# Performance work log

Measured on AMD Instinct MI355X. Metric: run time of the kernel, lower is better.

The kernel has to match this reference:

```python
import jax, jax.numpy as jnp
import numpy as np

N = 50000      # entity nodes
E = 300000     # edges in edge_index_all (and edge_index)
E_LINE = 50000 # line-graph edges over relations
EH = 128       # e_hidden
RH = 64        # r_hidden
REL1 = 2000
REL2 = 2000
GH = 3 * EH + RH  # GAT hidden = 448


def seg_softmax(e, idx, n):
    # torch_geometric softmax: exp(e - segmax[idx]) / (segsum + 1e-16)
    m = jax.ops.segment_max(e, idx, num_segments=n)
    ex = jnp.exp(e - m[idx])
    s = jax.ops.segment_sum(ex, idx, num_segments=n)
    return ex / (s[idx] + 1e-16)


def setup_inputs() -> dict:
    key = jax.random.key(0)
    ks = jax.random.split(key, 24)

    def nrm(k, shape, s=0.1):
        return jax.random.normal(k, shape, dtype=jnp.float32) * s

    # edges without self loops: dst = (src + off) % N, off in [1, N)
    src = jax.random.randint(ks[0], (E,), 0, N)
    off = jax.random.randint(ks[1], (E,), 1, N)
    edge_index_all = jnp.stack([src, (src + off) % N])
    src2 = jax.random.randint(ks[2], (E,), 0, N)
    off2 = jax.random.randint(ks[3], (E,), 1, N)
    edge_index = jnp.stack([src2, (src2 + off2) % N])

    rel = jax.random.randint(ks[4], (E,), 0, REL1)
    rel_all = jax.random.randint(ks[5], (E,), 0, 2 * REL1)
    line_graph_index_out = jax.random.randint(ks[6], (2, E_LINE), 0, REL1)
    line_graph_index_in = jax.random.randint(ks[7], (2, E_LINE), 0, REL1)

    return {
        "x_e": nrm(ks[8], (N, EH), 1.0),
        "rel_emb1": nrm(ks[9], (REL1, RH), 1.0),
        "rel_emb2": nrm(ks[10], (REL2, RH), 1.0),
        "w_gcn1": nrm(ks[11], (EH, EH)),
        "Wh1": nrm(ks[12], (EH, EH)),
        "bh1": nrm(ks[13], (EH,)),
        "w_gcn2": nrm(ks[14], (EH, EH)),
        "Wh2": nrm(ks[15], (EH, EH)),
        "bh2": nrm(ks[16], (EH,)),
        "ai_l": nrm(ks[17], (RH,)),
        "aj_l": nrm(ks[18], (RH,)),
        "w_tw": nrm(ks[19], (2 * EH + RH,)),
        "ai_g": nrm(ks[20], (GH,)),
        "aj_g": nrm(ks[21], (GH,)),
        "ar_g": nrm(ks[22], (RH,)),
        "edge_index": edge_index,
        "rel": rel,
        "edge_index_all": edge_index_all,
        "rel_all": rel_all,
        "line_graph_index_out": line_graph_index_out,
        "line_graph_index_in": line_graph_index_in,
    }


def mrea_forward(x_e, rel_emb1, w_gcn1, Wh1, bh1, w_gcn2, Wh2, bh2,
                 ai_l, aj_l, w_tw, ai_g, aj_g, ar_g,
                 edge_index_all, rel_all, lg_out, lg_in):
    n = x_e.shape[0]
    # GCN/GAT unpack: edge_index_j, edge_index_i = edge_index (row0=j, row1=i)
    j, i = edge_index_all[0], edge_index_all[1]

    def gcn(x, W):
        deg = jax.ops.segment_sum(jnp.ones(i.shape, x.dtype), i, num_segments=n)
        dinv = jnp.where(deg > 0, deg ** -0.5, 0.0)
        norm = dinv[j] * dinv[i]  # [E]
        agg = jax.nn.relu(jax.ops.segment_sum(norm[:, None] * x[j], i, num_segments=n))
        return agg @ W.T

    def highway(x1, x2, W, b):
        g = jax.nn.sigmoid(x1 @ W.T + b)
        return g * x2 + (1.0 - g) * x1

    x = highway(x_e, gcn(x_e, w_gcn1), Wh1, bh1)
    x = highway(x, gcn(x, w_gcn2), Wh2, bh2)

    # L_GAT over relation line graphs (softmax grouped by edge_index_j, as in source)
    nr = rel_emb1.shape[0]
    def l_gat(xr, ei):
        jj, ii = ei[0], ei[1]
        e = (xr @ ai_l)[ii] + (xr @ aj_l)[jj]
        alpha = seg_softmax(jax.nn.leaky_relu(e), jj, nr)
        return jax.nn.relu(jax.ops.segment_sum(alpha[:, None] * xr[jj], ii, num_segments=nr))

    rel_emb = jnp.concatenate([l_gat(rel_emb1, lg_out), l_gat(rel_emb1, lg_in)], axis=0)  # [2*REL1, RH]

    # T-wise attention: edge_index_i, edge_index_j = edge_index_all (row0=i, row1=j)
    ti, tj = edge_index_all[0], edge_index_all[1]
    feat = jnp.concatenate([x[ti], rel_emb[rel_all], x[tj]], axis=1)  # [E, 2e+r]
    att = seg_softmax(feat @ w_tw, ti, n)
    x_agg = jax.nn.relu(jax.ops.segment_sum(feat * att[:, None], ti, num_segments=n))
    x_rel = jnp.concatenate([x, x_agg], axis=1)  # [N, 3e+r]

    # GAT on x_rel with relation bias (row0=j, row1=i)
    e = (x_rel @ ai_g)[i] + (x_rel @ aj_g)[j] + (rel_emb @ ar_g)[rel_all]
    alpha = seg_softmax(jax.nn.leaky_relu(e), i, n)
    gat_out = jax.nn.relu(jax.ops.segment_sum(alpha[:, None] * x_rel[j], i, num_segments=n))

    return jnp.concatenate([x_rel, gat_out], axis=1)  # [N, 2*(3e+r)]


def reference(x_e, rel_emb1, rel_emb2, w_gcn1, Wh1, bh1, w_gcn2, Wh2, bh2,
              ai_l, aj_l, w_tw, ai_g, aj_g, ar_g,
              edge_index, rel, edge_index_all, rel_all,
              line_graph_index_out, line_graph_index_in):
    # Branch rel.max()+1 == rel1_size is true for our data -> rel_emb1 used.
    # rel_emb2, edge_index, rel do not enter the computation on this branch.
    return mrea_forward(x_e, rel_emb1, w_gcn1, Wh1, bh1, w_gcn2, Wh2, bh2,
                        ai_l, aj_l, w_tw, ai_g, aj_g, ar_g,
                        edge_index_all, rel_all,
                        line_graph_index_out, line_graph_index_in)
```

## Files before the change

kernel.cpp:

```cpp
#include <hip/hip_runtime.h>
#include <math.h>

#define NN 50000
#define EE 300000
#define EL 50000
#define EH 128
#define RH 64
#define R1 2000
#define NR2 4000
#define OD 896
#define NT64 782
#define GCNB 12500
#define CAP 32
#define LGCAP 64

using f32x4 = __attribute__((ext_vector_type(4))) float;
using bf16x8 = __attribute__((ext_vector_type(8))) short;

__device__ __forceinline__ float leaky(float x) { return x >= 0.f ? x : 0.01f * x; }

__device__ __forceinline__ void atomicMaxF(float* addr, float val) {
    if (val >= 0.f) atomicMax((int*)addr, __float_as_int(val));
    else            atomicMin((unsigned int*)addr, __float_as_uint(val));
}

__device__ __forceinline__ short bfrn(float f) {
    unsigned u = __float_as_uint(f);
    return (short)((u + 0x7FFFu + ((u >> 16) & 1u)) >> 16);
}
__device__ __forceinline__ void cvt1(float f, short& h, short& l) {
    h = bfrn(f);
    float hf = __uint_as_float(((unsigned)(unsigned short)h) << 16);
    l = bfrn(f - hf);
}
__device__ __forceinline__ void cvt8(float4 a, float4 b, bf16x8& hi, bf16x8& lo) {
    float v[8] = {a.x, a.y, a.z, a.w, b.x, b.y, b.z, b.w};
#pragma unroll
    for (int e = 0; e < 8; ++e) {
        short h, l;
        cvt1(v[e], h, l);
        hi[e] = h;
        lo[e] = l;
    }
}

__device__ __forceinline__ float2 bf2f(unsigned u) {
    float2 f;
    f.x = __uint_as_float(u << 16);
    f.y = __uint_as_float(u & 0xFFFF0000u);
    return f;
}
__device__ __forceinline__ float bf1f(unsigned short u) {
    return __uint_as_float(((unsigned)u) << 16);
}
__device__ __forceinline__ unsigned packbf(float a, float b) {
    return (unsigned)(unsigned short)bfrn(a) | (((unsigned)(unsigned short)bfrn(b)) << 16);
}

__global__ __launch_bounds__(256) void k_sij(const float* __restrict__ rel1,
                                             const float* __restrict__ ai_l, const float* __restrict__ aj_l,
                                             float* __restrict__ s_i, float* __restrict__ s_j) {
    int r = blockIdx.x * 256 + threadIdx.x;
    if (r < R1) {
        const float* m = rel1 + (long)r * 64;
        float a = 0.f, bb = 0.f;
#pragma unroll
        for (int c = 0; c < 64; ++c) {
            float v = m[c];
            a += v * ai_l[c];
            bb += v * aj_l[c];
        }
        s_i[r] = a;
        s_j[r] = bb;
    }
}

__global__ void k_fill_all(const int* __restrict__ e0, const int* __restrict__ e1,
                           const int* __restrict__ rel_all,
                           int* __restrict__ cnt0, int* __restrict__ cnt1,
                           int2* __restrict__ csr0p, int2* __restrict__ csr1p,
                           const int* __restrict__ lgo, const int* __restrict__ lgi,
                           const float* __restrict__ s_i, const float* __restrict__ s_j,
                           float* __restrict__ lgsc, float* __restrict__ lgmax,
                           int* __restrict__ lgcnt, int* __restrict__ lgsrc,
                           int* __restrict__ lgpos,
                           const float* __restrict__ W0, const float* __restrict__ W1,
                           const float* __restrict__ W2, const float* __restrict__ W3,
                           float* __restrict__ P0, float* __restrict__ P1,
                           float* __restrict__ P2, float* __restrict__ P3) {
    if (blockIdx.x < 32) {
        int slot = blockIdx.x * 256 + threadIdx.x;
        int m = slot >> 11;
        int rem = slot & 2047;
        int kb = rem >> 9;
        int nt = (rem >> 6) & 7;
        int l = rem & 63;
        const float* W = m == 0 ? W0 : m == 1 ? W1 : m == 2 ? W2 : W3;
        float* P = m == 0 ? P0 : m == 1 ? P1 : m == 2 ? P2 : P3;
        int n = (nt << 4) + (l & 15);
        int k0 = (kb << 5) + ((l >> 4) << 2);
        float4 a0 = *(const float4*)(W + (n << 7) + k0);
        float4 a1 = *(const float4*)(W + (n << 7) + k0 + 16);
        bf16x8 hv, lv;
        cvt8(a0, a1, hv, lv);
        int u = ((kb << 3) + nt) * 64 + l;
        *(bf16x8*)(P + ((long)u << 2)) = hv;
        *(bf16x8*)(P + 8192 + ((long)u << 2)) = lv;
        return;
    }
    int gid = (blockIdx.x - 32) * blockDim.x + threadIdx.x;
    int stride = (gridDim.x - 32) * blockDim.x;
    for (int i = gid; i < EE; i += stride) {
        int j0 = e0[i], i1 = e1[i], ra = rel_all[i];
        int p = atomicAdd(&cnt0[j0], 1);
        if (p < CAP) csr0p[(j0 << 5) + p] = make_int2(i1, ra);
        int q = atomicAdd(&cnt1[i1], 1);
        if (q < CAP) csr1p[(i1 << 5) + q] = make_int2(j0, ra);
    }
    for (int e = gid; e < 2 * EL; e += stride) {
        int g1 = e >= EL;
        int ee = g1 ? e - EL : e;
        const int* L = g1 ? lgi : lgo;
        int jj = L[ee], ii = L[ee + EL];
        float v = leaky(s_j[jj] + s_i[ii]);
        lgsc[e] = v;
        atomicMaxF(&lgmax[(g1 ? R1 : 0) + jj], v);
        int g = (g1 ? R1 : 0) + ii;
        int p = atomicAdd(&lgcnt[g], 1);
        if (p < LGCAP) {
            lgsrc[(g << 6) + p] = jj;
            lgpos[e] = (g << 6) + p;
        } else {
            lgpos[e] = -1;
        }
    }
}

template <bool RELU>
__device__ __forceinline__ void mfma_phase(const float* __restrict__ A, const float* __restrict__ P,
                                           float4* lds4, int tid, int l, int arow, f32x4 (&acc)[8]) {
#pragma unroll
    for (int s = 0; s < 2; ++s) {
        const float* Ap = A + ((long)arow << 7) + (s << 6) + ((l >> 4) << 2);
        float4 a0 = *(const float4*)(Ap);
        float4 a1 = *(const float4*)(Ap + 16);
        float4 a2 = *(const float4*)(Ap + 32);
        float4 a3 = *(const float4*)(Ap + 48);
        if (RELU) {
            a0.x = fmaxf(a0.x, 0.f); a0.y = fmaxf(a0.y, 0.f); a0.z = fmaxf(a0.z, 0.f); a0.w = fmaxf(a0.w, 0.f);
            a1.x = fmaxf(a1.x, 0.f); a1.y = fmaxf(a1.y, 0.f); a1.z = fmaxf(a1.z, 0.f); a1.w = fmaxf(a1.w, 0.f);
            a2.x = fmaxf(a2.x, 0.f); a2.y = fmaxf(a2.y, 0.f); a2.z = fmaxf(a2.z, 0.f); a2.w = fmaxf(a2.w, 0.f);
            a3.x = fmaxf(a3.x, 0.f); a3.y = fmaxf(a3.y, 0.f); a3.z = fmaxf(a3.z, 0.f); a3.w = fmaxf(a3.w, 0.f);
        }
        __syncthreads();
        const float4* srcH = (const float4*)P + (s << 10);
        const float4* srcL = (const float4*)P + 2048 + (s << 10);
#pragma unroll
        for (int i = 0; i < 4; ++i) {
            lds4[(i << 8) + tid] = srcH[(i << 8) + tid];
            lds4[1024 + (i << 8) + tid] = srcL[(i << 8) + tid];
        }
        __syncthreads();
        bf16x8 ah0, al0, ah1, al1;
        cvt8(a0, a1, ah0, al0);
        cvt8(a2, a3, ah1, al1);
        const bf16x8* BH = (const bf16x8*)lds4;
        const bf16x8* BL = BH + 1024;
#pragma unroll
        for (int nt = 0; nt < 8; ++nt) {
            bf16x8 bh0 = BH[(nt << 6) + l];
            bf16x8 bl0 = BL[(nt << 6) + l];
            bf16x8 bh1 = BH[512 + (nt << 6) + l];
            bf16x8 bl1 = BL[512 + (nt << 6) + l];
            f32x4 c = acc[nt];
            c = __builtin_amdgcn_mfma_f32_16x16x32_bf16(ah0, bh0, c, 0, 0, 0);
            c = __builtin_amdgcn_mfma_f32_16x16x32_bf16(al0, bh0, c, 0, 0, 0);
            c = __builtin_amdgcn_mfma_f32_16x16x32_bf16(ah0, bl0, c, 0, 0, 0);
            c = __builtin_amdgcn_mfma_f32_16x16x32_bf16(ah1, bh1, c, 0, 0, 0);
            c = __builtin_amdgcn_mfma_f32_16x16x32_bf16(al1, bh1, c, 0, 0, 0);
            c = __builtin_amdgcn_mfma_f32_16x16x32_bf16(ah1, bl1, c, 0, 0, 0);
            acc[nt] = c;
        }
    }
}

template <bool XB>
__global__ __launch_bounds__(256) void k_gcn_mfma(const float* __restrict__ Agg, const float* __restrict__ Xin,
                                                  float* __restrict__ Xout,
                                                  const float* __restrict__ Pg, const float* __restrict__ Ph,
                                                  const float* __restrict__ b,
                                                  const float* __restrict__ wtw192, float* __restrict__ xb,
                                                  unsigned short* __restrict__ xm) {
    __shared__ float4 lds4[2048];
    const int tid = threadIdx.x;
    const int l = tid & 63;
    const int wv = tid >> 6;
    const int l15 = l & 15;
    const int l4 = l >> 4;
    const int rowbase = blockIdx.x * 64 + (wv << 4);
    int arow = rowbase + l15;
    if (arow >= NN) arow = NN - 1;
    f32x4 tAcc[8], hAcc[8];
#pragma unroll
    for (int nt = 0; nt < 8; ++nt) {
        tAcc[nt] = {0.f, 0.f, 0.f, 0.f};
        hAcc[nt] = {0.f, 0.f, 0.f, 0.f};
    }
    mfma_phase<true>(Agg, Pg, lds4, tid, l, arow, tAcc);
    mfma_phase<false>(Xin, Ph, lds4, tid, l, arow, hAcc);
    const int r0 = rowbase + (l4 << 2);
    float xbp[4] = {0.f, 0.f, 0.f, 0.f};
#pragma unroll
    for (int nt = 0; nt < 8; ++nt) {
        float bv = b[(nt << 4) + l15];
#pragma unroll
        for (int r = 0; r < 4; ++r) {
            int row = r0 + r;
            if (row < NN) {
                long off = ((long)row << 7) + (nt << 4) + l15;
                float xv = Xin[off];
                float g = 1.f / (1.f + expf(-(hAcc[nt][r] + bv)));
                float ov = g * tAcc[nt][r] + (1.f - g) * xv;
                Xout[off] = ov;
                if (XB) {
                    xbp[r] += ov * wtw192[(nt << 4) + l15];
                    xm[off] = (unsigned short)bfrn(ov);
                }
            }
        }
    }
    if (XB) {
#pragma unroll
        for (int r = 0; r < 4; ++r) {
#pragma unroll
            for (int off = 1; off < 16; off <<= 1) xbp[r] += __shfl_xor(xbp[r], off);
            int row = r0 + r;
            if (l15 == 0 && row < NN) xb[row] = xbp[r];
        }
    }
}

template <int MODE>
__global__ __launch_bounds__(256) void k_gcn_gather(const int2* __restrict__ csr1p, const int* __restrict__ cnt1,
                                                    const float* __restrict__ x, float* __restrict__ agg,
                                                    const int* __restrict__ lgo, const int* __restrict__ lgi,
                                                    const float* __restrict__ lgsc, const float* __restrict__ lgmax,
                                                    float* __restrict__ lgsum,
                                                    const int* __restrict__ lgpos, float* __restrict__ lgscp,
                                                    const int* __restrict__ lgcnt, const int* __restrict__ lgsrc,
                                                    const float* __restrict__ rel1, float* __restrict__ relemb,
                                                    const float* __restrict__ wtw, const float* __restrict__ arg,
                                                    float* __restrict__ rw, float* __restrict__ gr) {
    if (blockIdx.x < GCNB) {
        int w = blockIdx.x * 4 + (threadIdx.x >> 6);
        int lane = threadIdx.x & 63;
        int cw = cnt1[w];
        int deg = cw > CAP ? CAP : cw;
        int b = w << 5;
        float dd = cw > 0 ? rsqrtf((float)cw) : 0.f;
        int sidx = 0;
        float wt = 0.f;
        if (lane < deg) {
            sidx = csr1p[b + lane].x;
            int cs = cnt1[sidx];
            wt = dd * (cs > 0 ? rsqrtf((float)cs) : 0.f);
        }
        const float2* x2 = (const float2*)x;
        float2 aA = {0.f, 0.f}, aB = {0.f, 0.f}, aC = {0.f, 0.f}, aD = {0.f, 0.f};
        int j = 0;
        for (; j + 3 < deg; j += 4) {
            int s0 = __shfl(sidx, j), s1 = __shfl(sidx, j + 1);
            int s2 = __shfl(sidx, j + 2), s3 = __shfl(sidx, j + 3);
            float w0 = __shfl(wt, j), w1 = __shfl(wt, j + 1);
            float w2 = __shfl(wt, j + 2), w3 = __shfl(wt, j + 3);
            float2 v0 = x2[((long)s0 << 6) + lane];
            float2 v1 = x2[((long)s1 << 6) + lane];
            float2 v2 = x2[((long)s2 << 6) + lane];
            float2 v3 = x2[((long)s3 << 6) + lane];
            aA.x += w0 * v0.x; aA.y += w0 * v0.y;
            aB.x += w1 * v1.x; aB.y += w1 * v1.y;
            aC.x += w2 * v2.x; aC.y += w2 * v2.y;
            aD.x += w3 * v3.x; aD.y += w3 * v3.y;
        }
        for (; j < deg; ++j) {
            int s0 = __shfl(sidx, j);
            float w0 = __shfl(wt, j);
            float2 v0 = x2[((long)s0 << 6) + lane];
            aA.x += w0 * v0.x; aA.y += w0 * v0.y;
        }
        float2 r;
        r.x = (aA.x + aB.x) + (aC.x + aD.x);
        r.y = (aA.y + aB.y) + (aC.y + aD.y);
        ((float2*)agg)[((long)w << 6) + lane] = r;
        return;
    }
    if (MODE == 1) {
        int gid = (blockIdx.x - GCNB) * 256 + threadIdx.x;
        const int stride = 391 * 256;
        for (int e = gid; e < 2 * EL; e += stride) {
            int g1 = e >= EL;
            int ee = g1 ? e - EL : e;
            const int* L = g1 ? lgi : lgo;
            int jjg = (g1 ? R1 : 0) + L[ee];
            float ex = expf(lgsc[e] - lgmax[jjg]);
            int lp = lgpos[e];
            if (lp >= 0) lgscp[lp] = ex;
            atomicAdd(&lgsum[jjg], ex);
        }
    } else {
        int d = (blockIdx.x - GCNB) * 4 + (threadIdx.x >> 6);
        int lane = threadIdx.x & 63;
        if (d >= NR2) return;
        int base = d >= R1 ? R1 : 0;
        int cd = lgcnt[d];
        int deg = cd > LGCAP ? LGCAP : cd;
        int b = d << 6;
        int src = 0;
        float al = 0.f;
        if (lane < deg) {
            src = lgsrc[b + lane];
            al = lgscp[b + lane] / (lgsum[base + src] + 1e-16f);
        }
        float aA = 0.f, aB = 0.f;
        int j = 0;
        for (; j + 1 < deg; j += 2) {
            float a0 = __shfl(al, j), a1 = __shfl(al, j + 1);
            int s0 = __shfl(src, j), s1 = __shfl(src, j + 1);
            aA += a0 * rel1[((long)s0 << 6) + lane];
            aB += a1 * rel1[((long)s1 << 6) + lane];
        }
        if (j < deg) {
            float a0 = __shfl(al, j);
            int s0 = __shfl(src, j);
            aA += a0 * rel1[((long)s0 << 6) + lane];
        }
        float v = fmaxf(aA + aB, 0.f);
        relemb[((long)d << 6) + lane] = v;
        float pa = v * wtw[128 + lane];
        float pb = v * arg[lane];
        for (int off = 32; off > 0; off >>= 1) {
            pa += __shfl_down(pa, off);
            pb += __shfl_down(pb, off);
        }
        if (lane == 0) { rw[d] = pa; gr[d] = pb; }
    }
}

__global__ __launch_bounds__(256) void k_tw_gather(const int2* __restrict__ csr0p, const int* __restrict__ cnt0,
                                                   const float* __restrict__ xb, const float* __restrict__ rw,
                                                   const float* __restrict__ x, const unsigned short* __restrict__ xm,
                                                   const float* __restrict__ relemb,
                                                   const float* __restrict__ aig, const float* __restrict__ ajg,
                                                   float* __restrict__ out,
                                                   float* __restrict__ ga, float* __restrict__ gb,
                                                   unsigned short* __restrict__ ym) {
    int w = (blockIdx.x * blockDim.x + threadIdx.x) >> 6;
    int lane = threadIdx.x & 63;
    if (w >= NN) return;
    int cw = cnt0[w];
    int deg = cw > CAP ? CAP : cw;
    int b = w << 5;
    int trx = 0, trr = 0;
    float v = -INFINITY;
    if (lane < deg) {
        int2 tr = csr0p[b + lane];
        trx = tr.x; trr = tr.y;
        v = xb[trx] + rw[trr];
    }
    float m = v;
#pragma unroll
    for (int off = 32; off > 0; off >>= 1) m = fmaxf(m, __shfl_xor(m, off));
    float al = (lane < deg) ? expf(v - m) : 0.f;
    float sum = al;
#pragma unroll
    for (int off = 32; off > 0; off >>= 1) sum += __shfl_xor(sum, off);
    const float2* x2 = (const float2*)x;
    int c2 = 2 * lane;
    float2 xt = x2[((long)w << 6) + lane];
    float a2A = 0.f, a2B = 0.f;
    float2 a3A = {0.f, 0.f}, a3B = {0.f, 0.f};
    int j = 0;
    for (; j + 3 < deg; j += 4) {
        float al0 = __shfl(al, j), al1 = __shfl(al, j + 1);
        float al2 = __shfl(al, j + 2), al3 = __shfl(al, j + 3);
        int x0i = __shfl(trx, j), x1i = __shfl(trx, j + 1);
        int x2i = __shfl(trx, j + 2), x3i = __shfl(trx, j + 3);
        int y0i = __shfl(trr, j), y1i = __shfl(trr, j + 1);
        int y2i = __shfl(trr, j + 2), y3i = __shfl(trr, j + 3);
        float r0 = relemb[((long)y0i << 6) + lane];
        float r1 = relemb[((long)y1i << 6) + lane];
        float r2 = relemb[((long)y2i << 6) + lane];
        float r3 = relemb[((long)y3i << 6) + lane];
        float2 v0 = bf2f(*(const unsigned*)(xm + ((long)x0i << 7) + c2));
        float2 v1 = bf2f(*(const unsigned*)(xm + ((long)x1i << 7) + c2));
        float2 v2 = bf2f(*(const unsigned*)(xm + ((long)x2i << 7) + c2));
        float2 v3 = bf2f(*(const unsigned*)(xm + ((long)x3i << 7) + c2));
        a2A += al0 * r0 + al1 * r1;
        a2B += al2 * r2 + al3 * r3;
        a3A.x += al0 * v0.x + al1 * v1.x;  a3A.y += al0 * v0.y + al1 * v1.y;
        a3B.x += al2 * v2.x + al3 * v3.x;  a3B.y += al2 * v2.y + al3 * v3.y;
    }
    for (; j < deg; ++j) {
        float alA = __shfl(al, j);
        int xA = __shfl(trx, j);
        int yA = __shfl(trr, j);
        a2A += alA * relemb[((long)yA << 6) + lane];
        float2 xvA = bf2f(*(const unsigned*)(xm + ((long)xA << 7) + c2));
        a3A.x += alA * xvA.x; a3A.y += alA * xvA.y;
    }
    float r = 1.f / (sum + 1e-16f);
    float sr = sum * r;
    float2 v23;
    v23.x = fmaxf(xt.x * sr, 0.f);
    v23.y = fmaxf(xt.y * sr, 0.f);
    float v4 = fmaxf((a2A + a2B) * r, 0.f);
    float2 v56;
    v56.x = fmaxf((a3A.x + a3B.x) * r, 0.f);
    v56.y = fmaxf((a3A.y + a3B.y) * r, 0.f);
    float* o = out + (long)w * OD;
    *(float2*)(o + c2) = xt;
    *(float2*)(o + 128 + c2) = v23;
    o[256 + lane] = v4;
    *(float2*)(o + 320 + c2) = v56;
    unsigned short* yr = ym + (long)w * 192;
    yr[lane] = (unsigned short)bfrn(v4);
    *(unsigned*)(yr + 64 + c2) = packbf(v56.x, v56.y);
    float da = xt.x * aig[c2] + xt.y * aig[c2 + 1] + v23.x * aig[128 + c2] + v23.y * aig[129 + c2] +
               v4 * aig[256 + lane] + v56.x * aig[320 + c2] + v56.y * aig[321 + c2];
    float db = xt.x * ajg[c2] + xt.y * ajg[c2 + 1] + v23.x * ajg[128 + c2] + v23.y * ajg[129 + c2] +
               v4 * ajg[256 + lane] + v56.x * ajg[320 + c2] + v56.y * ajg[321 + c2];
    for (int off = 32; off > 0; off >>= 1) {
        da += __shfl_down(da, off);
        db += __shfl_down(db, off);
    }
    if (lane == 0) { ga[w] = da; gb[w] = db; }
}

__global__ __launch_bounds__(256) void k_gat_gather(const int2* __restrict__ csr1p, const int* __restrict__ cnt1,
                                                    const float* __restrict__ ga, const float* __restrict__ gb,
                                                    const float* __restrict__ gr,
                                                    const unsigned short* __restrict__ xm,
                                                    const unsigned short* __restrict__ ym,
                                                    float* __restrict__ out) {
    int w = (blockIdx.x * blockDim.x + threadIdx.x) >> 6;
    int lane = threadIdx.x & 63;
    if (w >= NN) return;
    int cw = cnt1[w];
    int deg = cw > CAP ? CAP : cw;
    int b = w << 5;
    float gaw = ga[w];
    int px = 0;
    float v = -INFINITY;
    if (lane < deg) {
        int2 p = csr1p[b + lane];
        px = p.x;
        v = leaky(gaw + gb[px] + gr[p.y]);
    }
    float m = v;
#pragma unroll
    for (int off = 32; off > 0; off >>= 1) m = fmaxf(m, __shfl_xor(m, off));
    float al = (lane < deg) ? expf(v - m) : 0.f;
    float sum = al;
#pragma unroll
    for (int off = 32; off > 0; off >>= 1) sum += __shfl_xor(sum, off);
    int c2 = 2 * lane;
    float2 c0A = {0.f, 0.f}, c0B = {0.f, 0.f};
    float2 c2A = {0.f, 0.f}, c2B = {0.f, 0.f};
    float  c4A = 0.f, c4B = 0.f;
    float2 c5A = {0.f, 0.f}, c5B = {0.f, 0.f};
    int j = 0;
    for (; j + 3 < deg; j += 4) {
        float al0 = __shfl(al, j), al1 = __shfl(al, j + 1);
        float al2 = __shfl(al, j + 2), al3 = __shfl(al, j + 3);
        int p0 = __shfl(px, j), p1 = __shfl(px, j + 1);
        int p2 = __shfl(px, j + 2), p3 = __shfl(px, j + 3);
        const unsigned short* y0 = ym + (long)p0 * 192;
        const unsigned short* y1 = ym + (long)p1 * 192;
        const unsigned short* y2 = ym + (long)p2 * 192;
        const unsigned short* y3 = ym + (long)p3 * 192;
        float2 x0 = bf2f(*(const unsigned*)(xm + ((long)p0 << 7) + c2));
        float2 x1v = bf2f(*(const unsigned*)(xm + ((long)p1 << 7) + c2));
        float2 x2v = bf2f(*(const unsigned*)(xm + ((long)p2 << 7) + c2));
        float2 x3v = bf2f(*(const unsigned*)(xm + ((long)p3 << 7) + c2));
        float yv0 = bf1f(y0[lane]), yv1 = bf1f(y1[lane]);
        float yv2 = bf1f(y2[lane]), yv3 = bf1f(y3[lane]);
        float2 z0 = bf2f(*(const unsigned*)(y0 + 64 + c2));
        float2 z1 = bf2f(*(const unsigned*)(y1 + 64 + c2));
        float2 z2 = bf2f(*(const unsigned*)(y2 + 64 + c2));
        float2 z3 = bf2f(*(const unsigned*)(y3 + 64 + c2));
        c0A.x += al0 * x0.x + al1 * x1v.x;   c0A.y += al0 * x0.y + al1 * x1v.y;
        c0B.x += al2 * x2v.x + al3 * x3v.x;  c0B.y += al2 * x2v.y + al3 * x3v.y;
        c2A.x += al0 * fmaxf(x0.x, 0.f) + al1 * fmaxf(x1v.x, 0.f);
        c2A.y += al0 * fmaxf(x0.y, 0.f) + al1 * fmaxf(x1v.y, 0.f);
        c2B.x += al2 * fmaxf(x2v.x, 0.f) + al3 * fmaxf(x3v.x, 0.f);
        c2B.y += al2 * fmaxf(x2v.y, 0.f) + al3 * fmaxf(x3v.y, 0.f);
        c4A += al0 * yv0 + al1 * yv1;
        c4B += al2 * yv2 + al3 * yv3;
        c5A.x += al0 * z0.x + al1 * z1.x;  c5A.y += al0 * z0.y + al1 * z1.y;
        c5B.x += al2 * z2.x + al3 * z3.x;  c5B.y += al2 * z2.y + al3 * z3.y;
    }
    for (; j < deg; ++j) {
        float al0 = __shfl(al, j);
        int p0 = __shfl(px, j);
        const unsigned short* y0 = ym + (long)p0 * 192;
        float2 xv = bf2f(*(const unsigned*)(xm + ((long)p0 << 7) + c2));
        float yv = bf1f(y0[lane]);
        float2 zv = bf2f(*(const unsigned*)(y0 + 64 + c2));
        c0B.x += al0 * xv.x; c0B.y += al0 * xv.y;
        c2B.x += al0 * fmaxf(xv.x, 0.f); c2B.y += al0 * fmaxf(xv.y, 0.f);
        c4B += al0 * yv;
        c5B.x += al0 * zv.x; c5B.y += al0 * zv.y;
    }
    float r = 1.f / (sum + 1e-16f);
    float* o = out + (long)w * OD + 448;
    float2 w0, w2, w5;
    w0.x = fmaxf((c0A.x + c0B.x) * r, 0.f);
    w0.y = fmaxf((c0A.y + c0B.y) * r, 0.f);
    w2.x = fmaxf((c2A.x + c2B.x) * r, 0.f);
    w2.y = fmaxf((c2A.y + c2B.y) * r, 0.f);
    w5.x = fmaxf((c5A.x + c5B.x) * r, 0.f);
    w5.y = fmaxf((c5A.y + c5B.y) * r, 0.f);
    *(float2*)(o + c2) = w0;
    *(float2*)(o + 128 + c2) = w2;
    o[256 + lane] = fmaxf((c4A + c4B) * r, 0.f);
    *(float2*)(o + 320 + c2) = w5;
}

static inline int gs(long n) {
    long b = (n + 255) / 256;
    return (int)(b > 8192 ? 8192 : b);
}

extern "C" void kernel_launch(void* const* d_in, const int* in_sizes, int n_in,
                              void* d_out, int out_size, void* d_ws, size_t ws_size,
                              hipStream_t stream) {
    (void)in_sizes; (void)n_in; (void)out_size; (void)ws_size;

    const float* x_e   = (const float*)d_in[0];
    const float* rel1  = (const float*)d_in[1];
    const float* wgcn1 = (const float*)d_in[3];
    const float* Wh1   = (const float*)d_in[4];
    const float* bh1   = (const float*)d_in[5];
    const float* wgcn2 = (const float*)d_in[6];
    const float* Wh2   = (const float*)d_in[7];
    const float* bh2   = (const float*)d_in[8];
    const float* ai_l  = (const float*)d_in[9];
    const float* aj_l  = (const float*)d_in[10];
    const float* w_tw  = (const float*)d_in[11];
    const float* ai_g  = (const float*)d_in[12];
    const float* aj_g  = (const float*)d_in[13];
    const float* ar_g  = (const float*)d_in[14];
    const int* eia     = (const int*)d_in[17];
    const int* rel_all = (const int*)d_in[18];
    const int* lgo     = (const int*)d_in[19];
    const int* lgi     = (const int*)d_in[20];

    const int* e0 = eia;
    const int* e1 = eia + EE;

    float* out = (float*)d_out;
    float* ws  = (float*)d_ws;

    float* x1     = ws + 0;
    float* agg    = ws + 6400000;
    float* relemb = ws + 12800000;
    float* lgsum  = ws + 13056000;
    int*   cnt0   = (int*)(ws + 13060000);
    int*   cnt1   = (int*)(ws + 13110000);
    int*   lgcnt  = (int*)(ws + 13160000);
    float* lgmax  = ws + 13164000;
    float* xb     = ws + 13218000;
    float* rw     = ws + 13268000;
    float* gr     = ws + 13272000;
    float* ga     = ws + 13276000;
    float* gb     = ws + 13326000;
    int2*  csr0p  = (int2*)(ws + 13376000);
    int2*  csr1p  = (int2*)(ws + 16576000);
    float* wt1    = ws + 19776000;
    float* wt2    = ws + 19792384;
    float* wt3    = ws + 19808768;
    float* wt4    = ws + 19825152;
    float* s_i    = ws + 19841536;
    float* s_j    = ws + 19843536;
    float* lgsc   = ws + 19845536;
    float* lgscp  = ws + 19945536;
    int*   lgsrc  = (int*)(ws + 20201536);
    int*   lgpos  = (int*)(ws + 20457536);
    unsigned short* xm = (unsigned short*)(ws + 20557536);
    unsigned short* ym = (unsigned short*)(ws + 23757536);

    hipMemsetAsync(lgsum, 0, (size_t)112000 * sizeof(float), stream);
    k_sij<<<8, 256, 0, stream>>>(rel1, ai_l, aj_l, s_i, s_j);

    k_fill_all<<<gs(EE) + 32, 256, 0, stream>>>(e0, e1, rel_all, cnt0, cnt1, csr0p, csr1p,
                                                lgo, lgi, s_i, s_j, lgsc, lgmax, lgcnt, lgsrc, lgpos,
                                                wgcn1, Wh1, wgcn2, Wh2, wt1, wt2, wt3, wt4);

    k_gcn_gather<1><<<GCNB + 391, 256, 0, stream>>>(csr1p, cnt1, x_e, agg,
                                                    lgo, lgi, lgsc, lgmax, lgsum,
                                                    lgpos, lgscp, lgcnt, lgsrc, rel1, relemb,
                                                    w_tw, ar_g, rw, gr);
    k_gcn_mfma<false><<<NT64, 256, 0, stream>>>(agg, x_e, x1, wt1, wt2, bh1, nullptr, nullptr, nullptr);

    k_gcn_gather<2><<<GCNB + 1000, 256, 0, stream>>>(csr1p, cnt1, x1, agg,
                                                     lgo, lgi, lgsc, lgmax, lgsum,
                                                     lgpos, lgscp, lgcnt, lgsrc, rel1, relemb,
                                                     w_tw, ar_g, rw, gr);
    k_gcn_mfma<true><<<NT64, 256, 0, stream>>>(agg, x1, x1, wt3, wt4, bh2, w_tw + 192, xb, xm);

    k_tw_gather<<<12500, 256, 0, stream>>>(csr0p, cnt0, xb, rw, x1, xm, relemb, ai_g, aj_g, out, ga, gb, ym);

    k_gat_gather<<<12500, 256, 0, stream>>>(csr1p, cnt1, ga, gb, gr, xm, ym, out);
}
```

Before: 317.6 us.

## Fuse memset into pre-kernel, move csr0 build into gather, bf16 relemb, 512-thread blocks

Replaces the memset plus s_ij kernel with one kernel that also zeroes the lgsum region. Moves the csr0 CSR construction out of the fill kernel into extra blocks of the first GCN gather, so it overlaps with the gather work. Stores the relation embedding as bf16 to shrink the gather reads in the triple-wise kernel. Doubles block size to 512 threads (8 waves) for the gather kernels. The bf16 relation embedding adds rounding error, and the larger blocks may change occupancy.

```diff
diff --git a/kernel.cpp b/kernel.cpp
--- a/kernel.cpp
+++ b/kernel.cpp
@@ -10,7 +10,10 @@
 #define NR2 4000
 #define OD 896
 #define NT64 782
-#define GCNB 12500
+#define GB 6250
+#define LG1B 196
+#define C0B 600
+#define LG2B 500
 #define CAP 32
 #define LGCAP 64
 
@@ -57,28 +60,34 @@
     return (unsigned)(unsigned short)bfrn(a) | (((unsigned)(unsigned short)bfrn(b)) << 16);
 }
 
-__global__ __launch_bounds__(256) void k_sij(const float* __restrict__ rel1,
-                                             const float* __restrict__ ai_l, const float* __restrict__ aj_l,
-                                             float* __restrict__ s_i, float* __restrict__ s_j) {
-    int r = blockIdx.x * 256 + threadIdx.x;
-    if (r < R1) {
-        const float* m = rel1 + (long)r * 64;
-        float a = 0.f, bb = 0.f;
-#pragma unroll
-        for (int c = 0; c < 64; ++c) {
-            float v = m[c];
-            a += v * ai_l[c];
-            bb += v * aj_l[c];
-        }
-        s_i[r] = a;
-        s_j[r] = bb;
-    }
+__global__ __launch_bounds__(256) void k_pre0(const float* __restrict__ rel1,
+                                              const float* __restrict__ ai_l, const float* __restrict__ aj_l,
+                                              float* __restrict__ s_i, float* __restrict__ s_j,
+                                              float* __restrict__ zbase) {
+    int b = blockIdx.x, tid = threadIdx.x;
+    if (b < 8) {
+        int r = b * 256 + tid;
+        if (r < R1) {
+            const float* m = rel1 + (long)r * 64;
+            float a = 0.f, bb = 0.f;
+#pragma unroll
+            for (int c = 0; c < 64; ++c) {
+                float v = m[c];
+                a += v * ai_l[c];
+                bb += v * aj_l[c];
+            }
+            s_i[r] = a;
+            s_j[r] = bb;
+        }
+        return;
+    }
+    int idx = (b - 8) * 1024 + tid * 4;
+    if (idx < 112000) *(float4*)(zbase + idx) = make_float4(0.f, 0.f, 0.f, 0.f);
 }
 
 __global__ void k_fill_all(const int* __restrict__ e0, const int* __restrict__ e1,
                            const int* __restrict__ rel_all,
-                           int* __restrict__ cnt0, int* __restrict__ cnt1,
-                           int2* __restrict__ csr0p, int2* __restrict__ csr1p,
+                           int* __restrict__ cnt1, int2* __restrict__ csr1p,
                            const int* __restrict__ lgo, const int* __restrict__ lgi,
                            const float* __restrict__ s_i, const float* __restrict__ s_j,
                            float* __restrict__ lgsc, float* __restrict__ lgmax,
@@ -112,8 +121,6 @@
     int stride = (gridDim.x - 32) * blockDim.x;
     for (int i = gid; i < EE; i += stride) {
         int j0 = e0[i], i1 = e1[i], ra = rel_all[i];
-        int p = atomicAdd(&cnt0[j0], 1);
-        if (p < CAP) csr0p[(j0 << 5) + p] = make_int2(i1, ra);
         int q = atomicAdd(&cnt1[i1], 1);
         if (q < CAP) csr1p[(i1 << 5) + q] = make_int2(j0, ra);
     }
@@ -241,18 +248,21 @@
 }
 
 template <int MODE>
-__global__ __launch_bounds__(256) void k_gcn_gather(const int2* __restrict__ csr1p, const int* __restrict__ cnt1,
+__global__ __launch_bounds__(512) void k_gcn_gather(const int2* __restrict__ csr1p, const int* __restrict__ cnt1,
                                                     const float* __restrict__ x, float* __restrict__ agg,
                                                     const int* __restrict__ lgo, const int* __restrict__ lgi,
                                                     const float* __restrict__ lgsc, const float* __restrict__ lgmax,
                                                     float* __restrict__ lgsum,
                                                     const int* __restrict__ lgpos, float* __restrict__ lgscp,
                                                     const int* __restrict__ lgcnt, const int* __restrict__ lgsrc,
-                                                    const float* __restrict__ rel1, float* __restrict__ relemb,
+                                                    const float* __restrict__ rel1, unsigned short* __restrict__ rm,
                                                     const float* __restrict__ wtw, const float* __restrict__ arg,
-                                                    float* __restrict__ rw, float* __restrict__ gr) {
-    if (blockIdx.x < GCNB) {
-        int w = blockIdx.x * 4 + (threadIdx.x >> 6);
+                                                    float* __restrict__ rw, float* __restrict__ gr,
+                                                    const int* __restrict__ e0, const int* __restrict__ e1,
+                                                    const int* __restrict__ rel_all,
+                                                    int* __restrict__ cnt0, int2* __restrict__ csr0p) {
+    if (blockIdx.x < GB) {
+        int w = blockIdx.x * 8 + (threadIdx.x >> 6);
         int lane = threadIdx.x & 63;
         int cw = cnt1[w];
         int deg = cw > CAP ? CAP : cw;
@@ -295,20 +305,28 @@
         return;
     }
     if (MODE == 1) {
-        int gid = (blockIdx.x - GCNB) * 256 + threadIdx.x;
-        const int stride = 391 * 256;
-        for (int e = gid; e < 2 * EL; e += stride) {
-            int g1 = e >= EL;
-            int ee = g1 ? e - EL : e;
-            const int* L = g1 ? lgi : lgo;
-            int jjg = (g1 ? R1 : 0) + L[ee];
-            float ex = expf(lgsc[e] - lgmax[jjg]);
-            int lp = lgpos[e];
-            if (lp >= 0) lgscp[lp] = ex;
-            atomicAdd(&lgsum[jjg], ex);
+        if (blockIdx.x < GB + LG1B) {
+            int e = (blockIdx.x - GB) * 512 + threadIdx.x;
+            if (e < 2 * EL) {
+                int g1 = e >= EL;
+                int ee = g1 ? e - EL : e;
+                const int* L = g1 ? lgi : lgo;
+                int jjg = (g1 ? R1 : 0) + L[ee];
+                float ex = expf(lgsc[e] - lgmax[jjg]);
+                int lp = lgpos[e];
+                if (lp >= 0) lgscp[lp] = ex;
+                atomicAdd(&lgsum[jjg], ex);
+            }
+        } else {
+            int i = (blockIdx.x - GB - LG1B) * 512 + threadIdx.x;
+            if (i < EE) {
+                int j0 = e0[i], i1 = e1[i], ra = rel_all[i];
+                int p = atomicAdd(&cnt0[j0], 1);
+                if (p < CAP) csr0p[(j0 << 5) + p] = make_int2(i1, ra);
+            }
         }
     } else {
-        int d = (blockIdx.x - GCNB) * 4 + (threadIdx.x >> 6);
+        int d = (blockIdx.x - GB) * 8 + (threadIdx.x >> 6);
         int lane = threadIdx.x & 63;
         if (d >= NR2) return;
         int base = d >= R1 ? R1 : 0;
@@ -335,7 +353,7 @@
             aA += a0 * rel1[((long)s0 << 6) + lane];
         }
         float v = fmaxf(aA + aB, 0.f);
-        relemb[((long)d << 6) + lane] = v;
+        rm[(d << 6) + lane] = (unsigned short)bfrn(v);
         float pa = v * wtw[128 + lane];
         float pb = v * arg[lane];
         for (int off = 32; off > 0; off >>= 1) {
@@ -346,10 +364,10 @@
     }
 }
 
-__global__ __launch_bounds__(256) void k_tw_gather(const int2* __restrict__ csr0p, const int* __restrict__ cnt0,
+__global__ __launch_bounds__(512) void k_tw_gather(const int2* __restrict__ csr0p, const int* __restrict__ cnt0,
                                                    const float* __restrict__ xb, const float* __restrict__ rw,
                                                    const float* __restrict__ x, const unsigned short* __restrict__ xm,
-                                                   const float* __restrict__ relemb,
+                                                   const unsigned short* __restrict__ rm,
                                                    const float* __restrict__ aig, const float* __restrict__ ajg,
                                                    float* __restrict__ out,
                                                    float* __restrict__ ga, float* __restrict__ gb,
@@ -387,10 +405,10 @@
         int x2i = __shfl(trx, j + 2), x3i = __shfl(trx, j + 3);
         int y0i = __shfl(trr, j), y1i = __shfl(trr, j + 1);
         int y2i = __shfl(trr, j + 2), y3i = __shfl(trr, j + 3);
-        float r0 = relemb[((long)y0i << 6) + lane];
-        float r1 = relemb[((long)y1i << 6) + lane];
-        float r2 = relemb[((long)y2i << 6) + lane];
-        float r3 = relemb[((long)y3i << 6) + lane];
+        float r0 = bf1f(rm[(y0i << 6) + lane]);
+        float r1 = bf1f(rm[(y1i << 6) + lane]);
+        float r2 = bf1f(rm[(y2i << 6) + lane]);
+        float r3 = bf1f(rm[(y3i << 6) + lane]);
         float2 v0 = bf2f(*(const unsigned*)(xm + ((long)x0i << 7) + c2));
         float2 v1 = bf2f(*(const unsigned*)(xm + ((long)x1i << 7) + c2));
         float2 v2 = bf2f(*(const unsigned*)(xm + ((long)x2i << 7) + c2));
@@ -404,7 +422,7 @@
         float alA = __shfl(al, j);
         int xA = __shfl(trx, j);
         int yA = __shfl(trr, j);
-        a2A += alA * relemb[((long)yA << 6) + lane];
+        a2A += alA * bf1f(rm[(yA << 6) + lane]);
         float2 xvA = bf2f(*(const unsigned*)(xm + ((long)xA << 7) + c2));
         a3A.x += alA * xvA.x; a3A.y += alA * xvA.y;
     }
@@ -436,7 +454,7 @@
     if (lane == 0) { ga[w] = da; gb[w] = db; }
 }
 
-__global__ __launch_bounds__(256) void k_gat_gather(const int2* __restrict__ csr1p, const int* __restrict__ cnt1,
+__global__ __launch_bounds__(512) void k_gat_gather(const int2* __restrict__ csr1p, const int* __restrict__ cnt1,
                                                     const float* __restrict__ ga, const float* __restrict__ gb,
                                                     const float* __restrict__ gr,
                                                     const unsigned short* __restrict__ xm,
@@ -563,7 +581,7 @@
 
     float* x1     = ws + 0;
     float* agg    = ws + 6400000;
-    float* relemb = ws + 12800000;
+    unsigned short* rm = (unsigned short*)(ws + 12800000);
     float* lgsum  = ws + 13056000;
     int*   cnt0   = (int*)(ws + 13060000);
     int*   cnt1   = (int*)(ws + 13110000);
@@ -589,26 +607,27 @@
     unsigned short* xm = (unsigned short*)(ws + 20557536);
     unsigned short* ym = (unsigned short*)(ws + 23757536);
 
-    hipMemsetAsync(lgsum, 0, (size_t)112000 * sizeof(float), stream);
-    k_sij<<<8, 256, 0, stream>>>(rel1, ai_l, aj_l, s_i, s_j);
-
-    k_fill_all<<<gs(EE) + 32, 256, 0, stream>>>(e0, e1, rel_all, cnt0, cnt1, csr0p, csr1p,
+    k_pre0<<<118, 256, 0, stream>>>(rel1, ai_l, aj_l, s_i, s_j, lgsum);
+
+    k_fill_all<<<gs(EE) + 32, 256, 0, stream>>>(e0, e1, rel_all, cnt1, csr1p,
                                                 lgo, lgi, s_i, s_j, lgsc, lgmax, lgcnt, lgsrc, lgpos,
                                                 wgcn1, Wh1, wgcn2, Wh2, wt1, wt2, wt3, wt4);
 
-    k_gcn_gather<1><<<GCNB + 391, 256, 0, stream>>>(csr1p, cnt1, x_e, agg,
-                                                    lgo, lgi, lgsc, lgmax, lgsum,
-                                                    lgpos, lgscp, lgcnt, lgsrc, rel1, relemb,
-                                                    w_tw, ar_g, rw, gr);
+    k_gcn_gather<1><<<GB + LG1B + C0B, 512, 0, stream>>>(csr1p, cnt1, x_e, agg,
+                                                         lgo, lgi, lgsc, lgmax, lgsum,
+                                                         lgpos, lgscp, lgcnt, lgsrc, rel1, rm,
+                                                         w_tw, ar_g, rw, gr,
+                                                         e0, e1, rel_all, cnt0, csr0p);
     k_gcn_mfma<false><<<NT64, 256, 0, stream>>>(agg, x_e, x1, wt1, wt2, bh1, nullptr, nullptr, nullptr);
 
-    k_gcn_gather<2><<<GCNB + 1000, 256, 0, stream>>>(csr1p, cnt1, x1, agg,
-                                                     lgo, lgi, lgsc, lgmax, lgsum,
-                                                     lgpos, lgscp, lgcnt, lgsrc, rel1, relemb,
-                                                     w_tw, ar_g, rw, gr);
+    k_gcn_gather<2><<<GB + LG2B, 512, 0, stream>>>(csr1p, cnt1, x1, agg,
+                                                   lgo, lgi, lgsc, lgmax, lgsum,
+                                                   lgpos, lgscp, lgcnt, lgsrc, rel1, rm,
+                                                   w_tw, ar_g, rw, gr,
+                                                   e0, e1, rel_all, cnt0, csr0p);
     k_gcn_mfma<true><<<NT64, 256, 0, stream>>>(agg, x1, x1, wt3, wt4, bh2, w_tw + 192, xb, xm);
 
-    k_tw_gather<<<12500, 256, 0, stream>>>(csr0p, cnt0, xb, rw, x1, xm, relemb, ai_g, aj_g, out, ga, gb, ym);
-
-    k_gat_gather<<<12500, 256, 0, stream>>>(csr1p, cnt1, ga, gb, gr, xm, ym, out);
-}
+    k_tw_gather<<<GB, 512, 0, stream>>>(csr0p, cnt0, xb, rw, x1, xm, rm, ai_g, aj_g, out, ga, gb, ym);
+
+    k_gat_gather<<<GB, 512, 0, stream>>>(csr1p, cnt1, ga, gb, gr, xm, ym, out);
+}
```

Result: no change. 312.9 us (-1.5%).
